# Performance work log

Measured on AMD Instinct MI355X. Metric: run time of the kernel, lower is better.

Reference implementation:

```python
import jax, jax.numpy as jnp
import numpy as np
from jax import lax

B, L, EMB, C, H, NTF = 512, 1024, 4, 64, 64, 200
D2 = 2 * H  # 128, bi-LSTM feature dim


def setup_inputs() -> dict:
    key = jax.random.key(0)
    ks = iter(jax.random.split(key, 48))
    r = lambda shape, s=0.05: jax.random.normal(next(ks), shape, jnp.float32) * s
    inp = {"DNA_x": jax.random.normal(next(ks), (B, L, EMB), jnp.float32)}
    # conv stack: channels 4 -> 64 -> 64, kernel 8
    inp["conv0_w"] = r((C, EMB, 8)); inp["conv0_b"] = r((C,))
    inp["bn0_g"] = 1.0 + r((C,)); inp["bn0_b"] = r((C,))
    inp["bn0_m"] = r((C,)); inp["bn0_v"] = jax.random.uniform(next(ks), (C,), jnp.float32, 0.5, 1.5)
    inp["conv1_w"] = r((C, C, 8)); inp["conv1_b"] = r((C,))
    inp["bn1_g"] = 1.0 + r((C,)); inp["bn1_b"] = r((C,))
    inp["bn1_m"] = r((C,)); inp["bn1_v"] = jax.random.uniform(next(ks), (C,), jnp.float32, 0.5, 1.5)
    # bidirectional LSTM, torch gate order (i, f, g, o)
    for d in ("f", "b"):
        inp[f"wih_{d}"] = r((4 * H, C)); inp[f"whh_{d}"] = r((4 * H, H))
        inp[f"bih_{d}"] = r((4 * H,)); inp[f"bhh_{d}"] = r((4 * H,))
    # Bahdanau attention: W1, W2: 128->128, V: 128->NTF
    inp["W1_w"] = r((D2, D2)); inp["W1_b"] = r((D2,))
    inp["W2_w"] = r((D2, D2)); inp["W2_b"] = r((D2,))
    inp["V_w"] = r((NTF, D2)); inp["V_b"] = r((NTF,))
    # per-TF heads stacked: Linear(128->64), Linear(64->1)
    inp["fc1_w"] = r((NTF, 64, D2)); inp["fc1_b"] = r((NTF, 64))
    inp["fc2_w"] = r((NTF, 64)); inp["fc2_b"] = r((NTF,))
    return inp


def _conv(x, w, b):  # x:[B,Cin,L], w:[Cout,Cin,K]
    y = lax.conv_general_dilated(x, w, (1,), "VALID",
                                 dimension_numbers=("NCH", "OIH", "NCH"))
    return y + b[:, None]


def _bn(x, g, b, m, v):  # eval-mode BatchNorm1d over channel dim
    return (x - m[:, None]) * (g[:, None] / jnp.sqrt(v[:, None] + 1e-5)) + b[:, None]


def _lstm(x, Wih, Whh, bih, bhh):  # x:[B,T,D] -> ([B,T,H], h_T:[B,H])
    Bn = x.shape[0]
    Hh = Whh.shape[1]
    bias = bih + bhh
    def step(carry, xt):
        h, c = carry
        g = xt @ Wih.T + h @ Whh.T + bias
        i, f, gg, o = jnp.split(g, 4, axis=-1)
        c = jax.nn.sigmoid(f) * c + jax.nn.sigmoid(i) * jnp.tanh(gg)
        h = jax.nn.sigmoid(o) * jnp.tanh(c)
        return (h, c), h
    init = (jnp.zeros((Bn, Hh), x.dtype), jnp.zeros((Bn, Hh), x.dtype))
    (hT, _), hs = lax.scan(step, init, jnp.swapaxes(x, 0, 1))
    return jnp.swapaxes(hs, 0, 1), hT


def reference(DNA_x, conv0_w, conv0_b, bn0_g, bn0_b, bn0_m, bn0_v,
              conv1_w, conv1_b, bn1_g, bn1_b, bn1_m, bn1_v,
              wih_f, whh_f, bih_f, bhh_f, wih_b, whh_b, bih_b, bhh_b,
              W1_w, W1_b, W2_w, W2_b, V_w, V_b,
              fc1_w, fc1_b, fc2_w, fc2_b):
    x = jnp.swapaxes(DNA_x, 1, 2)                      # [B,EMB,L]
    x = jax.nn.relu(_bn(_conv(x, conv0_w, conv0_b), bn0_g, bn0_b, bn0_m, bn0_v))
    x = lax.reduce_window(x, -jnp.inf, lax.max, (1, 1, 4), (1, 1, 4), "VALID")
    x = jax.nn.relu(_bn(_conv(x, conv1_w, conv1_b), bn1_g, bn1_b, bn1_m, bn1_v))
    x = jnp.swapaxes(x, 1, 2)                          # [B,T,C], T=247
    hf, hTf = _lstm(x, wih_f, whh_f, bih_f, bhh_f)
    hb, hTb = _lstm(x[:, ::-1, :], wih_b, whh_b, bih_b, bhh_b)
    values = jnp.concatenate([hf, hb[:, ::-1, :]], axis=-1)   # [B,T,2H]
    # torch h_n.view(B, 2H) on [2,B,H]: flat reshape (replicated exactly)
    h_n = jnp.stack([hTf, hTb], axis=0).reshape(values.shape[0], -1)
    # Bahdanau attention with NTF query heads
    score = jnp.tanh(values @ W1_w.T + W1_b + (h_n @ W2_w.T + W2_b)[:, None, :]) @ V_w.T + V_b
    aw = jax.nn.softmax(score, axis=1)                 # [B,T,NTF], softmax over time
    context = jnp.einsum("btd,btk->bkd", values, aw)   # [B,NTF,2H]
    # fused per-TF MLP heads: grouped GEMM over NTF
    h1 = jax.nn.relu(jnp.einsum("bkd,kod->bko", context, fc1_w) + fc1_b)
    out = jnp.einsum("bko,ko->bk", h1, fc2_w) + fc2_b  # [B,NTF]
    return out
```

## Files before the change

kernel.cpp:

```cpp
#include <hip/hip_runtime.h>
#include <math.h>

#define BB 512
#define LL 1024
#define EMB 4
#define CC 64
#define NTF 200
#define TT 247
#define LP 254
#define D2 128

typedef __attribute__((ext_vector_type(8))) short short8;
typedef __attribute__((ext_vector_type(4))) float f32x4;
typedef __attribute__((ext_vector_type(4))) unsigned int uint4v;

__device__ __forceinline__ float sigf(float x) {
  return __builtin_amdgcn_rcpf(1.0f + __expf(-x));
}
__device__ __forceinline__ float tanhff(float x) {
  return 1.0f - 2.0f * __builtin_amdgcn_rcpf(__expf(2.0f * x) + 1.0f);
}

__device__ __forceinline__ void lds_barrier() {
  __builtin_amdgcn_s_waitcnt(0xC07F);
  __builtin_amdgcn_s_barrier();
}

__device__ __forceinline__ unsigned short bfr(float f) {
  unsigned u = __builtin_bit_cast(unsigned, f);
  u += 0x7fffu + ((u >> 16) & 1u);
  return (unsigned short)(u >> 16);
}

__global__ __launch_bounds__(256) void k_cvt(const float* __restrict__ w0,
    const float* __restrict__ w1,
    const float* __restrict__ wihf, const float* __restrict__ whhf,
    const float* __restrict__ wihb, const float* __restrict__ whhb,
    const float* __restrict__ bihf, const float* __restrict__ bhhf,
    const float* __restrict__ bihb, const float* __restrict__ bhhb,
    const float* __restrict__ W1w, const float* __restrict__ Vw,
    const float* __restrict__ f1w,
    unsigned short* __restrict__ wbf0, unsigned short* __restrict__ wbf1r,
    unsigned short* __restrict__ wihbf, unsigned short* __restrict__ whhbf,
    float* __restrict__ lbias,
    unsigned short* __restrict__ W1bf, unsigned short* __restrict__ Vbf,
    unsigned short* __restrict__ f1bf)
{
  int i = blockIdx.x * 256 + threadIdx.x;
  if (i < 2048) wbf0[i] = bfr(w0[i]);
  if (i < 32768) {
    int co = i >> 9, k = (i >> 6) & 7, ci = i & 63;
    wbf1r[i] = bfr(w1[co * 512 + ci * 8 + k]);
  }
  if (i < 16384) {
    wihbf[i] = bfr(wihf[i]);
    wihbf[16384 + i] = bfr(wihb[i]);
    whhbf[i] = bfr(whhf[i]);
    whhbf[16384 + i] = bfr(whhb[i]);
    W1bf[i] = bfr(W1w[i]);
  }
  if (i < 26624) {
    int row = i >> 7;
    Vbf[i] = (row < NTF) ? bfr(Vw[i]) : (unsigned short)0;
  }
  if (i < 256) {
    lbias[i] = bihf[i] + bhhf[i];
    lbias[256 + i] = bihb[i] + bhhb[i];
  }
  if (i < 1638400) f1bf[i] = bfr(f1w[i]);
}

__global__ __launch_bounds__(256) void k_conv0m(const float* __restrict__ x,
    const unsigned short* __restrict__ wbf0,
    const float* __restrict__ b0, const float* __restrict__ g0,
    const float* __restrict__ be0, const float* __restrict__ m0,
    const float* __restrict__ v0, unsigned short* __restrict__ pbf)
{
  int b = blockIdx.x, l0 = blockIdx.y * 64;
  __shared__ float xs[71 * 4];
  __shared__ float sc[64], sb[64];
  int tid = threadIdx.x;
  for (int j = tid; j < 71; j += 256) {
    int l = l0 + j;
    float4 xv = (l < LL) ? *(const float4*)(x + ((size_t)b * LL + l) * EMB)
                         : make_float4(0.f, 0.f, 0.f, 0.f);
    *(float4*)(xs + j * 4) = xv;
  }
  if (tid < 64) {
    float s = g0[tid] * rsqrtf(v0[tid] + 1e-5f);
    sc[tid] = s;
    sb[tid] = (b0[tid] - m0[tid]) * s + be0[tid];
  }
  __syncthreads();
  int w = tid >> 6, lane = tid & 63, nl = lane & 15, quad = lane >> 4;
  const float* ap = xs + (w * 16 + nl) * 4 + quad;
  short8 af;
  #pragma unroll
  for (int j = 0; j < 8; ++j) af[j] = (short)bfr(ap[j * 4]);
  f32x4 acc[4];
  #pragma unroll
  for (int nt = 0; nt < 4; ++nt) {
    short8 bf = __builtin_bit_cast(short8,
        *(const uint4v*)(wbf0 + ((nt * 16 + nl) * 32 + quad * 8)));
    acc[nt] = (f32x4){0.f, 0.f, 0.f, 0.f};
    acc[nt] = __builtin_amdgcn_mfma_f32_16x16x32_bf16(af, bf, acc[nt], 0, 0, 0);
  }
  int t = (l0 >> 2) + w * 4 + quad;
  if (t < LP) {
    #pragma unroll
    for (int nt = 0; nt < 4; ++nt) {
      int c = nt * 16 + nl;
      float scc = sc[c], sbc = sb[c];
      float mx = -1e30f;
      #pragma unroll
      for (int r = 0; r < 4; ++r) mx = fmaxf(mx, acc[nt][r] * scc + sbc);
      pbf[((size_t)b * LP + t) * CC + c] = bfr(fmaxf(mx, 0.0f));
    }
  }
}

__global__ __launch_bounds__(256) void k_conv1m(const unsigned short* __restrict__ pbf,
    const unsigned short* __restrict__ wbf1r,
    const float* __restrict__ b1, const float* __restrict__ g1,
    const float* __restrict__ be1, const float* __restrict__ m1,
    const float* __restrict__ v1, unsigned short* __restrict__ x2bf)
{
  int b = blockIdx.x, t0 = blockIdx.y * 64;
  __shared__ __align__(16) unsigned short ps[71 * 72];
  __shared__ float sc[64], sb[64];
  int tid = threadIdx.x;
  for (int j = tid; j < 71 * 32; j += 256) {
    int tl = j >> 5, cu = j & 31;
    int t = t0 + tl;
    unsigned v = (t < LP) ? *(const unsigned*)(pbf + ((size_t)b * LP + t) * CC + cu * 2) : 0u;
    *(unsigned*)(&ps[tl * 72 + cu * 2]) = v;
  }
  if (tid < 64) {
    float s = g1[tid] * rsqrtf(v1[tid] + 1e-5f);
    sc[tid] = s;
    sb[tid] = (b1[tid] - m1[tid]) * s + be1[tid];
  }
  __syncthreads();
  int w = tid >> 6, lane = tid & 63, nl = lane & 15, quad = lane >> 4;
  int tlb = w * 16 + nl;
  f32x4 acc[4];
  #pragma unroll
  for (int nt = 0; nt < 4; ++nt) acc[nt] = (f32x4){0.f, 0.f, 0.f, 0.f};
  #pragma unroll
  for (int k8 = 0; k8 < 8; ++k8) {
    short8 af0 = __builtin_bit_cast(short8,
        *(const uint4v*)(&ps[(tlb + k8) * 72 + 0 + quad * 8]));
    short8 af1 = __builtin_bit_cast(short8,
        *(const uint4v*)(&ps[(tlb + k8) * 72 + 32 + quad * 8]));
    #pragma unroll
    for (int nt = 0; nt < 4; ++nt) {
      int co = nt * 16 + nl;
      short8 bf0 = __builtin_bit_cast(short8,
          *(const uint4v*)(wbf1r + (size_t)co * 512 + k8 * 64 + 0 + quad * 8));
      short8 bf1 = __builtin_bit_cast(short8,
          *(const uint4v*)(wbf1r + (size_t)co * 512 + k8 * 64 + 32 + quad * 8));
      acc[nt] = __builtin_amdgcn_mfma_f32_16x16x32_bf16(af0, bf0, acc[nt], 0, 0, 0);
      acc[nt] = __builtin_amdgcn_mfma_f32_16x16x32_bf16(af1, bf1, acc[nt], 0, 0, 0);
    }
  }
  #pragma unroll
  for (int nt = 0; nt < 4; ++nt) {
    int c = nt * 16 + nl;
    float scc = sc[c], sbc = sb[c];
    #pragma unroll
    for (int r = 0; r < 4; ++r) {
      int t = t0 + w * 16 + quad * 4 + r;
      if (t < TT)
        x2bf[((size_t)b * TT + t) * CC + c] = bfr(fmaxf(acc[nt][r] * scc + sbc, 0.0f));
    }
  }
}

__global__ __launch_bounds__(256) void k_lstm_m(const unsigned short* __restrict__ x2bf,
    const unsigned short* __restrict__ wihbf, const unsigned short* __restrict__ whhbf,
    const float* __restrict__ lbias,
    unsigned short* __restrict__ values, float* __restrict__ hT)
{
  int b0 = blockIdx.x * 16;
  int dir = blockIdx.y;
  int tid = threadIdx.x;
  int w = tid >> 6, lane = tid & 63, l15 = lane & 15, quad = lane >> 4;
  int h0 = w * 16;
  const unsigned short* wih = wihbf + dir * 16384;
  const unsigned short* whh = whhbf + dir * 16384;

  short8 bx[4][2], bh[4][2];
  float bias_v[4];
  #pragma unroll
  for (int g = 0; g < 4; ++g) {
    int row = g * 64 + h0 + l15;
    #pragma unroll
    for (int k = 0; k < 2; ++k) {
      bx[g][k] = __builtin_bit_cast(short8, *(const uint4v*)(wih + row * 64 + k * 32 + quad * 8));
      bh[g][k] = __builtin_bit_cast(short8, *(const uint4v*)(whh + row * 64 + k * 32 + quad * 8));
    }
    bias_v[g] = lbias[dir * 256 + g * 64 + h0 + l15];
  }

  __shared__ __align__(16) unsigned short xls[2][8][16 * 72];
  __shared__ __align__(16) unsigned short hist[8][16 * 72];
  for (int j = tid; j < 16 * 72; j += 256) hist[7][j] = 0;

  int bl = tid >> 4, d4 = tid & 15;
  const unsigned short* xrow = x2bf + ((size_t)(b0 + bl) * TT) * 64 + d4 * 4;

  uint2 xr[8];
  #pragma unroll
  for (int k = 0; k < 8; ++k) {
    int t = dir ? (TT - 1 - k) : k;
    xr[k] = *(const uint2*)(xrow + (size_t)t * 64);
  }
  #pragma unroll
  for (int k = 0; k < 8; ++k)
    *(uint2*)(&xls[0][k][bl * 72 + d4 * 4]) = xr[k];
  #pragma unroll
  for (int k = 0; k < 8; ++k) {
    int s = 8 + k;
    int t = dir ? (TT - 1 - s) : s;
    xr[k] = *(const uint2*)(xrow + (size_t)t * 64);
  }
  __syncthreads();

  float cst[4] = {0.f, 0.f, 0.f, 0.f};
  for (int c = 0; c < 31; ++c) {
    int buf = c & 1;
    #pragma unroll
    for (int sl = 0; sl < 8; ++sl) {
      int hp = (sl + 7) & 7;
      short8 ax0 = __builtin_bit_cast(short8, *(const uint4v*)(&xls[buf][sl][l15 * 72 + quad * 8]));
      short8 ax1 = __builtin_bit_cast(short8, *(const uint4v*)(&xls[buf][sl][l15 * 72 + 32 + quad * 8]));
      short8 ah0 = __builtin_bit_cast(short8, *(const uint4v*)(&hist[hp][l15 * 72 + quad * 8]));
      short8 ah1 = __builtin_bit_cast(short8, *(const uint4v*)(&hist[hp][l15 * 72 + 32 + quad * 8]));
      f32x4 aX[4], aH[4];
      #pragma unroll
      for (int g = 0; g < 4; ++g) {
        aX[g] = (f32x4){bias_v[g], bias_v[g], bias_v[g], bias_v[g]};
        aX[g] = __builtin_amdgcn_mfma_f32_16x16x32_bf16(ax0, bx[g][0], aX[g], 0, 0, 0);
        aX[g] = __builtin_amdgcn_mfma_f32_16x16x32_bf16(ax1, bx[g][1], aX[g], 0, 0, 0);
        aH[g] = (f32x4){0.f, 0.f, 0.f, 0.f};
        aH[g] = __builtin_amdgcn_mfma_f32_16x16x32_bf16(ah0, bh[g][0], aH[g], 0, 0, 0);
        aH[g] = __builtin_amdgcn_mfma_f32_16x16x32_bf16(ah1, bh[g][1], aH[g], 0, 0, 0);
      }
      #pragma unroll
      for (int r = 0; r < 4; ++r) {
        float ig = sigf(aX[0][r] + aH[0][r]);
        float fg = sigf(aX[1][r] + aH[1][r]);
        float gg = tanhff(aX[2][r] + aH[2][r]);
        float og = sigf(aX[3][r] + aH[3][r]);
        cst[r] = fg * cst[r] + ig * gg;
        float hh = og * tanhff(cst[r]);
        hist[sl][(quad * 4 + r) * 72 + h0 + l15] = bfr(hh);
        if (c == 30 && sl == 6) {
          int bglob = b0 + quad * 4 + r;
          hT[((size_t)dir * BB + bglob) * 64 + h0 + l15] = hh;
        }
      }
      lds_barrier();
    }
    uint4v dv[4];
    #pragma unroll
    for (int i = 0; i < 4; ++i) {
      int flat = i * 256 + tid;
      int sl = flat >> 7, wb = (flat >> 3) & 15, c8 = flat & 7;
      dv[i] = *(const uint4v*)(&hist[sl][wb * 72 + c8 * 8]);
    }
    #pragma unroll
    for (int i = 0; i < 4; ++i) {
      int flat = i * 256 + tid;
      int sl = flat >> 7, wb = (flat >> 3) & 15, c8 = flat & 7;
      int s = c * 8 + sl;
      if (s < TT) {
        int t = dir ? (TT - 1 - s) : s;
        *(uint4v*)(values + ((size_t)(b0 + wb) * TT + t) * D2 + dir * 64 + c8 * 8) = dv[i];
      }
    }
    if (c < 30) {
      #pragma unroll
      for (int k = 0; k < 8; ++k)
        *(uint2*)(&xls[1 - buf][k][bl * 72 + d4 * 4]) = xr[k];
      #pragma unroll
      for (int k = 0; k < 8; ++k) {
        int s2 = (c + 2) * 8 + k;
        if (s2 > TT - 1) s2 = TT - 1;
        int t2 = dir ? (TT - 1 - s2) : s2;
        xr[k] = *(const uint2*)(xrow + (size_t)t2 * 64);
      }
    }
    lds_barrier();
  }
}

__global__ __launch_bounds__(128) void k_q2(const float* __restrict__ hT,
    const float* __restrict__ W2, const float* __restrict__ W2b,
    float* __restrict__ q2)
{
  int b = blockIdx.x;
  int tid = threadIdx.x;
  __shared__ float4 hn4[32];
  ((float*)hn4)[tid] = hT[(size_t)b * 128 + tid];
  __syncthreads();
  const float4* w4 = (const float4*)(W2 + (size_t)tid * 128);
  float a = W2b[tid];
  #pragma unroll
  for (int j = 0; j < 32; ++j) {
    float4 w = w4[j]; float4 h = hn4[j];
    a += w.x * h.x + w.y * h.y + w.z * h.z + w.w * h.w;
  }
  q2[(size_t)b * 128 + tid] = a;
}

__global__ __launch_bounds__(256) void k_score_m(const unsigned short* __restrict__ vbf,
    const unsigned short* __restrict__ W1bf, const float* __restrict__ W1b,
    const float* __restrict__ q2, const unsigned short* __restrict__ Vbf,
    const float* __restrict__ Vb, unsigned short* __restrict__ scoreT)
{
  int b = blockIdx.x, t0 = blockIdx.y * 64;
  int tid = threadIdx.x, w = tid >> 6, lane = tid & 63, l15 = lane & 15, quad = lane >> 4;
  __shared__ unsigned short us[64 * 136];
  __shared__ unsigned short sc2[64 * 213];
  const unsigned short* arow = vbf + ((size_t)b * TT + t0 + w * 16 + l15) * 128;
  short8 ax[4];
  #pragma unroll
  for (int ks = 0; ks < 4; ++ks)
    ax[ks] = __builtin_bit_cast(short8, *(const uint4v*)(arow + ks * 32 + quad * 8));
  #pragma unroll
  for (int nt = 0; nt < 8; ++nt) {
    int n = nt * 16 + l15;
    float base = W1b[n] + q2[(size_t)b * 128 + n];
    f32x4 acc = (f32x4){base, base, base, base};
    #pragma unroll
    for (int ks = 0; ks < 4; ++ks) {
      short8 bf = __builtin_bit_cast(short8,
          *(const uint4v*)(W1bf + (size_t)n * 128 + ks * 32 + quad * 8));
      acc = __builtin_amdgcn_mfma_f32_16x16x32_bf16(ax[ks], bf, acc, 0, 0, 0);
    }
    #pragma unroll
    for (int r = 0; r < 4; ++r)
      us[(w * 16 + quad * 4 + r) * 136 + nt * 16 + l15] = bfr(tanhff(acc[r]));
  }
  __syncthreads();
  short8 au[4];
  #pragma unroll
  for (int ks = 0; ks < 4; ++ks)
    au[ks] = __builtin_bit_cast(short8, *(const uint4v*)(&us[(w * 16 + l15) * 136 + ks * 32 + quad * 8]));
  for (int nt2 = 0; nt2 < 13; ++nt2) {
    int n = nt2 * 16 + l15;
    float b2 = (n < NTF) ? Vb[n] : 0.0f;
    f32x4 a2 = (f32x4){b2, b2, b2, b2};
    #pragma unroll
    for (int ks = 0; ks < 4; ++ks) {
      short8 bf = __builtin_bit_cast(short8,
          *(const uint4v*)(Vbf + (size_t)n * 128 + ks * 32 + quad * 8));
      a2 = __builtin_amdgcn_mfma_f32_16x16x32_bf16(au[ks], bf, a2, 0, 0, 0);
    }
    #pragma unroll
    for (int r = 0; r < 4; ++r) {
      int tl = w * 16 + quad * 4 + r;
      sc2[tl * 213 + n] = bfr(a2[r]);
    }
  }
  __syncthreads();
  int tg = tid & 3;
  #pragma unroll
  for (int pp = 0; pp < 4; ++pp) {
    int nrow = pp * 64 + (tid >> 2);
    if (nrow < NTF) {
      unsigned uu[8];
      #pragma unroll
      for (int k2 = 0; k2 < 8; ++k2) {
        unsigned lo = sc2[(tg * 16 + k2 * 2) * 213 + nrow];
        unsigned hi = sc2[(tg * 16 + k2 * 2 + 1) * 213 + nrow];
        uu[k2] = lo | (hi << 16);
      }
      size_t dst = ((size_t)b * 208 + nrow) * 256 + t0 + tg * 16;
      *(uint4v*)(scoreT + dst) = (uint4v){uu[0], uu[1], uu[2], uu[3]};
      *(uint4v*)(scoreT + dst + 8) = (uint4v){uu[4], uu[5], uu[6], uu[7]};
    }
  }
}

__global__ __launch_bounds__(256) void k_softmax(unsigned short* __restrict__ scoreT,
    float* __restrict__ sinv)
{
  int b = blockIdx.x, nc = blockIdx.y;
  int tid = threadIdx.x;
  int n = nc * 64 + (tid >> 2), tg = tid & 3;
  if (n >= NTF) return;
  unsigned short* row = scoreT + ((size_t)b * 208 + n) * 256 + tg * 64;
  uint4v ld[8];
  #pragma unroll
  for (int i = 0; i < 8; ++i) ld[i] = *(const uint4v*)(row + i * 8);
  float m = -1e30f;
  #pragma unroll
  for (int i = 0; i < 8; ++i) {
    #pragma unroll
    for (int u = 0; u < 4; ++u) {
      unsigned xv = ld[i][u];
      int t0 = tg * 64 + i * 8 + u * 2;
      float a = __builtin_bit_cast(float, xv << 16);
      float c = __builtin_bit_cast(float, xv & 0xffff0000u);
      if (t0 < TT) m = fmaxf(m, a);
      if (t0 + 1 < TT) m = fmaxf(m, c);
    }
  }
  m = fmaxf(m, __shfl_xor(m, 1, 64));
  m = fmaxf(m, __shfl_xor(m, 2, 64));
  float s = 0.0f;
  #pragma unroll
  for (int i = 0; i < 8; ++i) {
    uint4v ov;
    #pragma unroll
    for (int u = 0; u < 4; ++u) {
      unsigned xv = ld[i][u];
      int t0 = tg * 64 + i * 8 + u * 2;
      float a = __builtin_bit_cast(float, xv << 16);
      float c = __builtin_bit_cast(float, xv & 0xffff0000u);
      float ea = (t0 < TT) ? __expf(a - m) : 0.0f;
      float ec = (t0 + 1 < TT) ? __expf(c - m) : 0.0f;
      s += ea + ec;
      ov[u] = (unsigned)bfr(ea) | ((unsigned)bfr(ec) << 16);
    }
    *(uint4v*)(row + i * 8) = ov;
  }
  s += __shfl_xor(s, 1, 64);
  s += __shfl_xor(s, 2, 64);
  if (tg == 0) sinv[(size_t)b * NTF + n] = __builtin_amdgcn_rcpf(s);
}

__global__ __launch_bounds__(256) void k_ctx_m(const unsigned short* __restrict__ vbf,
    const unsigned short* __restrict__ scoreT, const float* __restrict__ sinv,
    unsigned short* __restrict__ ctxbf)
{
  int b = blockIdx.x;
  int tid = threadIdx.x, w = tid >> 6, lane = tid & 63, l15 = lane & 15, quad = lane >> 4;
  __shared__ __align__(16) unsigned short vt[128 * 264];
  __shared__ float sls[208];
  for (int flat = tid; flat < 247 * 64; flat += 256) {
    int t = flat >> 6, dp = flat & 63;
    unsigned v = *(const unsigned*)(vbf + ((size_t)b * TT + t) * D2 + dp * 2);
    vt[(dp * 2) * 264 + t] = (unsigned short)(v & 0xffffu);
    vt[(dp * 2 + 1) * 264 + t] = (unsigned short)(v >> 16);
  }
  for (int j = tid; j < 128 * 9; j += 256) {
    int d = j / 9, t = 247 + (j % 9);
    vt[d * 264 + t] = 0;
  }
  for (int j = tid; j < 208; j += 256) sls[j] = (j < NTF) ? sinv[(size_t)b * NTF + j] : 0.0f;
  __syncthreads();

  const unsigned short* abase = scoreT + (size_t)b * 208 * 256;
  for (int mi = 0; mi < 4; ++mi) {
    int mt = w + 4 * mi;
    if (mt >= 13) continue;
    const unsigned short* arow = abase + (size_t)(mt * 16 + l15) * 256;
    short8 af[8];
    #pragma unroll
    for (int ks = 0; ks < 8; ++ks)
      af[ks] = __builtin_bit_cast(short8, *(const uint4v*)(arow + ks * 32 + quad * 8));
    f32x4 acc[8];
    #pragma unroll
    for (int dt = 0; dt < 8; ++dt) {
      acc[dt] = (f32x4){0.f, 0.f, 0.f, 0.f};
      #pragma unroll
      for (int ks = 0; ks < 8; ++ks) {
        short8 bf = __builtin_bit_cast(short8,
            *(const uint4v*)(&vt[(dt * 16 + l15) * 264 + ks * 32 + quad * 8]));
        acc[dt] = __builtin_amdgcn_mfma_f32_16x16x32_bf16(af[ks], bf, acc[dt], 0, 0, 0);
      }
    }
    #pragma unroll
    for (int r = 0; r < 4; ++r) {
      int n = mt * 16 + quad * 4 + r;
      if (n < NTF) {
        float rs = sls[n];
        #pragma unroll
        for (int dt = 0; dt < 8; ++dt)
          ctxbf[((size_t)b * NTF + n) * D2 + dt * 16 + l15] = bfr(acc[dt][r] * rs);
      }
    }
  }
}

__global__ __launch_bounds__(256) void k_heads_m(const unsigned short* __restrict__ ctxbf,
    const unsigned short* __restrict__ f1bf, const float* __restrict__ fc1b,
    const float* __restrict__ fc2w, const float* __restrict__ fc2b,
    float* __restrict__ out)
{
  int n = blockIdx.x;
  int b0 = blockIdx.y * 128;
  int tid = threadIdx.x, w = tid >> 6, lane = tid & 63, l15 = lane & 15, quad = lane >> 4;
  short8 bfr_[4][4];
  float f1bv[4], f2v[4];
  #pragma unroll
  for (int nt = 0; nt < 4; ++nt) {
    int o = nt * 16 + l15;
    #pragma unroll
    for (int ks = 0; ks < 4; ++ks)
      bfr_[nt][ks] = __builtin_bit_cast(short8,
          *(const uint4v*)(f1bf + ((size_t)n * 64 + o) * 128 + ks * 32 + quad * 8));
    f1bv[nt] = fc1b[n * 64 + o];
    f2v[nt] = fc2w[n * 64 + o];
  }
  float f2b = fc2b[n];
  #pragma unroll
  for (int mi = 0; mi < 2; ++mi) {
    int m16 = (w * 2 + mi) * 16;
    const unsigned short* arow = ctxbf + ((size_t)(b0 + m16 + l15) * NTF + n) * 128;
    short8 af[4];
    #pragma unroll
    for (int ks = 0; ks < 4; ++ks)
      af[ks] = __builtin_bit_cast(short8, *(const uint4v*)(arow + ks * 32 + quad * 8));
    f32x4 acc[4];
    #pragma unroll
    for (int nt = 0; nt < 4; ++nt) {
      acc[nt] = (f32x4){0.f, 0.f, 0.f, 0.f};
      #pragma unroll
      for (int ks = 0; ks < 4; ++ks)
        acc[nt] = __builtin_amdgcn_mfma_f32_16x16x32_bf16(af[ks], bfr_[nt][ks], acc[nt], 0, 0, 0);
    }
    #pragma unroll
    for (int r = 0; r < 4; ++r) {
      float part = 0.0f;
      #pragma unroll
      for (int nt = 0; nt < 4; ++nt)
        part += fmaxf(acc[nt][r] + f1bv[nt], 0.0f) * f2v[nt];
      part += __shfl_xor(part, 1, 64);
      part += __shfl_xor(part, 2, 64);
      part += __shfl_xor(part, 4, 64);
      part += __shfl_xor(part, 8, 64);
      if (l15 == 0) {
        int bb = b0 + m16 + quad * 4 + r;
        out[(size_t)bb * NTF + n] = part + f2b;
      }
    }
  }
}

extern "C" void kernel_launch(void* const* d_in, const int* in_sizes, int n_in,
                              void* d_out, int out_size, void* d_ws, size_t ws_size,
                              hipStream_t stream)
{
  const float* x    = (const float*)d_in[0];
  const float* c0w  = (const float*)d_in[1];
  const float* c0b  = (const float*)d_in[2];
  const float* g0   = (const float*)d_in[3];
  const float* be0  = (const float*)d_in[4];
  const float* m0   = (const float*)d_in[5];
  const float* v0   = (const float*)d_in[6];
  const float* c1w  = (const float*)d_in[7];
  const float* c1b  = (const float*)d_in[8];
  const float* g1   = (const float*)d_in[9];
  const float* be1  = (const float*)d_in[10];
  const float* m1   = (const float*)d_in[11];
  const float* v1   = (const float*)d_in[12];
  const float* wihf = (const float*)d_in[13];
  const float* whhf = (const float*)d_in[14];
  const float* bihf = (const float*)d_in[15];
  const float* bhhf = (const float*)d_in[16];
  const float* wihb = (const float*)d_in[17];
  const float* whhb = (const float*)d_in[18];
  const float* bihb = (const float*)d_in[19];
  const float* bhhb = (const float*)d_in[20];
  const float* W1w  = (const float*)d_in[21];
  const float* W1b  = (const float*)d_in[22];
  const float* W2w  = (const float*)d_in[23];
  const float* W2b  = (const float*)d_in[24];
  const float* Vw   = (const float*)d_in[25];
  const float* Vb   = (const float*)d_in[26];
  const float* f1w  = (const float*)d_in[27];
  const float* f1b  = (const float*)d_in[28];
  const float* f2w  = (const float*)d_in[29];
  const float* f2b  = (const float*)d_in[30];

  float* ws = (float*)d_ws;
  unsigned short* scoreT = (unsigned short*)ws;
  unsigned short* pbf  = (unsigned short*)ws;
  unsigned short* x2bf = (unsigned short*)(ws + 8323072);
  unsigned short* vbf  = (unsigned short*)(ws + 25292800);
  float* hT     = ws + 33387520;
  float* q2     = ws + 33453056;
  float* sinv   = ws + 33518592;
  unsigned short* ctxbf = (unsigned short*)(ws + 33620992);
  unsigned short* wbf0  = (unsigned short*)(ws + 46728192);
  unsigned short* wbf1r = (unsigned short*)(ws + 46729216);
  unsigned short* wihbf = (unsigned short*)(ws + 46745600);
  unsigned short* whhbf = (unsigned short*)(ws + 46761984);
  float* lbias          = ws + 46778368;
  unsigned short* W1bf  = (unsigned short*)(ws + 46778880);
  unsigned short* Vbf   = (unsigned short*)(ws + 46787072);
  unsigned short* f1bf  = (unsigned short*)(ws + 46800384);
  float* out    = (float*)d_out;

  k_cvt<<<dim3(6400), 256, 0, stream>>>(c0w, c1w, wihf, whhf, wihb, whhb,
                                        bihf, bhhf, bihb, bhhb, W1w, Vw, f1w,
                                        wbf0, wbf1r, wihbf, whhbf, lbias, W1bf, Vbf, f1bf);
  k_conv0m<<<dim3(BB, 16), 256, 0, stream>>>(x, wbf0, c0b, g0, be0, m0, v0, pbf);
  k_conv1m<<<dim3(BB, 4), 256, 0, stream>>>(pbf, wbf1r, c1b, g1, be1, m1, v1, x2bf);
  k_lstm_m<<<dim3(BB / 16, 2), 256, 0, stream>>>(x2bf, wihbf, whhbf, lbias, vbf, hT);
  k_q2<<<dim3(BB), 128, 0, stream>>>(hT, W2w, W2b, q2);
  k_score_m<<<dim3(BB, 4), 256, 0, stream>>>(vbf, W1bf, W1b, q2, Vbf, Vb, scoreT);
  k_softmax<<<dim3(BB, 4), 256, 0, stream>>>(scoreT, sinv);
  k_ctx_m<<<dim3(BB), 256, 0, stream>>>(vbf, scoreT, sinv, ctxbf);
  k_heads_m<<<dim3(NTF, 4), 256, 0, stream>>>(ctxbf, f1bf, f1b, f2w, f2b, out);
}
```

Before: 514.9 us.

## Fuse softmax into context GEMM and merge LSTM directions into one block

The separate softmax kernel is removed. The score kernel now writes -inf padding for timesteps past the end, and the context kernel exponentiates the scores while loading them, sums each row with cross-lane shuffles, and scales the output by the reciprocal. The max subtraction is dropped, which relies on scores staying small enough for exp not to overflow. The LSTM now runs both directions in one 512-thread block with per-direction shared-memory buffers, using 4-step chunks instead of 8. This changes the chunk double-buffering and means each block runs 62 chunks instead of 31, with a barrier after every step.

```diff
diff --git a/kernel.cpp b/kernel.cpp
--- a/kernel.cpp
+++ b/kernel.cpp
@@ -176,15 +176,16 @@
   }
 }
 
-__global__ __launch_bounds__(256) void k_lstm_m(const unsigned short* __restrict__ x2bf,
+__global__ __launch_bounds__(512) void k_lstm_m(const unsigned short* __restrict__ x2bf,
     const unsigned short* __restrict__ wihbf, const unsigned short* __restrict__ whhbf,
     const float* __restrict__ lbias,
     unsigned short* __restrict__ values, float* __restrict__ hT)
 {
   int b0 = blockIdx.x * 16;
-  int dir = blockIdx.y;
   int tid = threadIdx.x;
-  int w = tid >> 6, lane = tid & 63, l15 = lane & 15, quad = lane >> 4;
+  int dir = tid >> 8;
+  int t256 = tid & 255;
+  int w = t256 >> 6, lane = tid & 63, l15 = lane & 15, quad = lane >> 4;
   int h0 = w * 16;
   const unsigned short* wih = wihbf + dir * 16384;
   const unsigned short* whh = whhbf + dir * 16384;
@@ -202,40 +203,39 @@
     bias_v[g] = lbias[dir * 256 + g * 64 + h0 + l15];
   }
 
-  __shared__ __align__(16) unsigned short xls[2][8][16 * 72];
-  __shared__ __align__(16) unsigned short hist[8][16 * 72];
-  for (int j = tid; j < 16 * 72; j += 256) hist[7][j] = 0;
-
-  int bl = tid >> 4, d4 = tid & 15;
+  __shared__ __align__(16) unsigned short xls[2][4][16 * 72];
+  __shared__ __align__(16) unsigned short hist[2][4][16 * 72];
+  for (int j = t256; j < 16 * 72; j += 256) hist[dir][3][j] = 0;
+
+  int bl = t256 >> 4, d4 = t256 & 15;
   const unsigned short* xrow = x2bf + ((size_t)(b0 + bl) * TT) * 64 + d4 * 4;
 
-  uint2 xr[8];
-  #pragma unroll
-  for (int k = 0; k < 8; ++k) {
+  uint2 xr[4];
+  #pragma unroll
+  for (int k = 0; k < 4; ++k) {
     int t = dir ? (TT - 1 - k) : k;
     xr[k] = *(const uint2*)(xrow + (size_t)t * 64);
   }
   #pragma unroll
-  for (int k = 0; k < 8; ++k)
-    *(uint2*)(&xls[0][k][bl * 72 + d4 * 4]) = xr[k];
-  #pragma unroll
-  for (int k = 0; k < 8; ++k) {
-    int s = 8 + k;
+  for (int k = 0; k < 4; ++k)
+    *(uint2*)(&xls[dir][k][bl * 72 + d4 * 4]) = xr[k];
+  #pragma unroll
+  for (int k = 0; k < 4; ++k) {
+    int s = 4 + k;
     int t = dir ? (TT - 1 - s) : s;
     xr[k] = *(const uint2*)(xrow + (size_t)t * 64);
   }
   __syncthreads();
 
   float cst[4] = {0.f, 0.f, 0.f, 0.f};
-  for (int c = 0; c < 31; ++c) {
-    int buf = c & 1;
-    #pragma unroll
-    for (int sl = 0; sl < 8; ++sl) {
-      int hp = (sl + 7) & 7;
-      short8 ax0 = __builtin_bit_cast(short8, *(const uint4v*)(&xls[buf][sl][l15 * 72 + quad * 8]));
-      short8 ax1 = __builtin_bit_cast(short8, *(const uint4v*)(&xls[buf][sl][l15 * 72 + 32 + quad * 8]));
-      short8 ah0 = __builtin_bit_cast(short8, *(const uint4v*)(&hist[hp][l15 * 72 + quad * 8]));
-      short8 ah1 = __builtin_bit_cast(short8, *(const uint4v*)(&hist[hp][l15 * 72 + 32 + quad * 8]));
+  for (int c = 0; c < 62; ++c) {
+    #pragma unroll
+    for (int sl = 0; sl < 4; ++sl) {
+      int hp = (sl + 3) & 3;
+      short8 ax0 = __builtin_bit_cast(short8, *(const uint4v*)(&xls[dir][sl][l15 * 72 + quad * 8]));
+      short8 ax1 = __builtin_bit_cast(short8, *(const uint4v*)(&xls[dir][sl][l15 * 72 + 32 + quad * 8]));
+      short8 ah0 = __builtin_bit_cast(short8, *(const uint4v*)(&hist[dir][hp][l15 * 72 + quad * 8]));
+      short8 ah1 = __builtin_bit_cast(short8, *(const uint4v*)(&hist[dir][hp][l15 * 72 + 32 + quad * 8]));
       f32x4 aX[4], aH[4];
       #pragma unroll
       for (int g = 0; g < 4; ++g) {
@@ -254,38 +254,38 @@
         float og = sigf(aX[3][r] + aH[3][r]);
         cst[r] = fg * cst[r] + ig * gg;
         float hh = og * tanhff(cst[r]);
-        hist[sl][(quad * 4 + r) * 72 + h0 + l15] = bfr(hh);
-        if (c == 30 && sl == 6) {
+        hist[dir][sl][(quad * 4 + r) * 72 + h0 + l15] = bfr(hh);
+        if (c == 61 && sl == 2) {
           int bglob = b0 + quad * 4 + r;
           hT[((size_t)dir * BB + bglob) * 64 + h0 + l15] = hh;
         }
       }
       lds_barrier();
     }
-    uint4v dv[4];
-    #pragma unroll
-    for (int i = 0; i < 4; ++i) {
-      int flat = i * 256 + tid;
+    uint4v dv[2];
+    #pragma unroll
+    for (int i = 0; i < 2; ++i) {
+      int flat = i * 256 + t256;
       int sl = flat >> 7, wb = (flat >> 3) & 15, c8 = flat & 7;
-      dv[i] = *(const uint4v*)(&hist[sl][wb * 72 + c8 * 8]);
-    }
-    #pragma unroll
-    for (int i = 0; i < 4; ++i) {
-      int flat = i * 256 + tid;
+      dv[i] = *(const uint4v*)(&hist[dir][sl][wb * 72 + c8 * 8]);
+    }
+    #pragma unroll
+    for (int i = 0; i < 2; ++i) {
+      int flat = i * 256 + t256;
       int sl = flat >> 7, wb = (flat >> 3) & 15, c8 = flat & 7;
-      int s = c * 8 + sl;
+      int s = c * 4 + sl;
       if (s < TT) {
         int t = dir ? (TT - 1 - s) : s;
         *(uint4v*)(values + ((size_t)(b0 + wb) * TT + t) * D2 + dir * 64 + c8 * 8) = dv[i];
       }
     }
-    if (c < 30) {
-      #pragma unroll
-      for (int k = 0; k < 8; ++k)
-        *(uint2*)(&xls[1 - buf][k][bl * 72 + d4 * 4]) = xr[k];
-      #pragma unroll
-      for (int k = 0; k < 8; ++k) {
-        int s2 = (c + 2) * 8 + k;
+    if (c < 61) {
+      #pragma unroll
+      for (int k = 0; k < 4; ++k)
+        *(uint2*)(&xls[dir][k][bl * 72 + d4 * 4]) = xr[k];
+      #pragma unroll
+      for (int k = 0; k < 4; ++k) {
+        int s2 = (c + 2) * 4 + k;
         if (s2 > TT - 1) s2 = TT - 1;
         int t2 = dir ? (TT - 1 - s2) : s2;
         xr[k] = *(const uint2*)(xrow + (size_t)t2 * 64);
@@ -373,8 +373,9 @@
       unsigned uu[8];
       #pragma unroll
       for (int k2 = 0; k2 < 8; ++k2) {
-        unsigned lo = sc2[(tg * 16 + k2 * 2) * 213 + nrow];
-        unsigned hi = sc2[(tg * 16 + k2 * 2 + 1) * 213 + nrow];
+        int ta = t0 + tg * 16 + k2 * 2;
+        unsigned lo = (ta < TT) ? (unsigned)sc2[(tg * 16 + k2 * 2) * 213 + nrow] : 0xFF80u;
+        unsigned hi = (ta + 1 < TT) ? (unsigned)sc2[(tg * 16 + k2 * 2 + 1) * 213 + nrow] : 0xFF80u;
         uu[k2] = lo | (hi << 16);
       }
       size_t dst = ((size_t)b * 208 + nrow) * 256 + t0 + tg * 16;
@@ -384,62 +385,13 @@
   }
 }
 
-__global__ __launch_bounds__(256) void k_softmax(unsigned short* __restrict__ scoreT,
-    float* __restrict__ sinv)
-{
-  int b = blockIdx.x, nc = blockIdx.y;
-  int tid = threadIdx.x;
-  int n = nc * 64 + (tid >> 2), tg = tid & 3;
-  if (n >= NTF) return;
-  unsigned short* row = scoreT + ((size_t)b * 208 + n) * 256 + tg * 64;
-  uint4v ld[8];
-  #pragma unroll
-  for (int i = 0; i < 8; ++i) ld[i] = *(const uint4v*)(row + i * 8);
-  float m = -1e30f;
-  #pragma unroll
-  for (int i = 0; i < 8; ++i) {
-    #pragma unroll
-    for (int u = 0; u < 4; ++u) {
-      unsigned xv = ld[i][u];
-      int t0 = tg * 64 + i * 8 + u * 2;
-      float a = __builtin_bit_cast(float, xv << 16);
-      float c = __builtin_bit_cast(float, xv & 0xffff0000u);
-      if (t0 < TT) m = fmaxf(m, a);
-      if (t0 + 1 < TT) m = fmaxf(m, c);
-    }
-  }
-  m = fmaxf(m, __shfl_xor(m, 1, 64));
-  m = fmaxf(m, __shfl_xor(m, 2, 64));
-  float s = 0.0f;
-  #pragma unroll
-  for (int i = 0; i < 8; ++i) {
-    uint4v ov;
-    #pragma unroll
-    for (int u = 0; u < 4; ++u) {
-      unsigned xv = ld[i][u];
-      int t0 = tg * 64 + i * 8 + u * 2;
-      float a = __builtin_bit_cast(float, xv << 16);
-      float c = __builtin_bit_cast(float, xv & 0xffff0000u);
-      float ea = (t0 < TT) ? __expf(a - m) : 0.0f;
-      float ec = (t0 + 1 < TT) ? __expf(c - m) : 0.0f;
-      s += ea + ec;
-      ov[u] = (unsigned)bfr(ea) | ((unsigned)bfr(ec) << 16);
-    }
-    *(uint4v*)(row + i * 8) = ov;
-  }
-  s += __shfl_xor(s, 1, 64);
-  s += __shfl_xor(s, 2, 64);
-  if (tg == 0) sinv[(size_t)b * NTF + n] = __builtin_amdgcn_rcpf(s);
-}
-
 __global__ __launch_bounds__(256) void k_ctx_m(const unsigned short* __restrict__ vbf,
-    const unsigned short* __restrict__ scoreT, const float* __restrict__ sinv,
+    const unsigned short* __restrict__ scoreT,
     unsigned short* __restrict__ ctxbf)
 {
   int b = blockIdx.x;
   int tid = threadIdx.x, w = tid >> 6, lane = tid & 63, l15 = lane & 15, quad = lane >> 4;
   __shared__ __align__(16) unsigned short vt[128 * 264];
-  __shared__ float sls[208];
   for (int flat = tid; flat < 247 * 64; flat += 256) {
     int t = flat >> 6, dp = flat & 63;
     unsigned v = *(const unsigned*)(vbf + ((size_t)b * TT + t) * D2 + dp * 2);
@@ -450,7 +402,6 @@
     int d = j / 9, t = 247 + (j % 9);
     vt[d * 264 + t] = 0;
   }
-  for (int j = tid; j < 208; j += 256) sls[j] = (j < NTF) ? sinv[(size_t)b * NTF + j] : 0.0f;
   __syncthreads();
 
   const unsigned short* abase = scoreT + (size_t)b * 208 * 256;
@@ -459,9 +410,26 @@
     if (mt >= 13) continue;
     const unsigned short* arow = abase + (size_t)(mt * 16 + l15) * 256;
     short8 af[8];
-    #pragma unroll
-    for (int ks = 0; ks < 8; ++ks)
-      af[ks] = __builtin_bit_cast(short8, *(const uint4v*)(arow + ks * 32 + quad * 8));
+    float ssum = 0.0f;
+    #pragma unroll
+    for (int ks = 0; ks < 8; ++ks) {
+      uint4v raw = *(const uint4v*)(arow + ks * 32 + quad * 8);
+      uint4v pk;
+      #pragma unroll
+      for (int u = 0; u < 4; ++u) {
+        unsigned xv = raw[u];
+        float a = __builtin_bit_cast(float, xv << 16);
+        float c2 = __builtin_bit_cast(float, xv & 0xffff0000u);
+        float ea = __expf(a);
+        float ec = __expf(c2);
+        ssum += ea + ec;
+        pk[u] = (unsigned)bfr(ea) | ((unsigned)bfr(ec) << 16);
+      }
+      af[ks] = __builtin_bit_cast(short8, pk);
+    }
+    ssum += __shfl_xor(ssum, 16, 64);
+    ssum += __shfl_xor(ssum, 32, 64);
+    float rs = __builtin_amdgcn_rcpf(ssum);
     f32x4 acc[8];
     #pragma unroll
     for (int dt = 0; dt < 8; ++dt) {
@@ -476,11 +444,11 @@
     #pragma unroll
     for (int r = 0; r < 4; ++r) {
       int n = mt * 16 + quad * 4 + r;
+      float rr = __shfl(rs, quad * 4 + r, 64);
       if (n < NTF) {
-        float rs = sls[n];
         #pragma unroll
         for (int dt = 0; dt < 8; ++dt)
-          ctxbf[((size_t)b * NTF + n) * D2 + dt * 16 + l15] = bfr(acc[dt][r] * rs);
+          ctxbf[((size_t)b * NTF + n) * D2 + dt * 16 + l15] = bfr(acc[dt][r] * rr);
       }
     }
   }
@@ -584,7 +552,6 @@
   unsigned short* vbf  = (unsigned short*)(ws + 25292800);
   float* hT     = ws + 33387520;
   float* q2     = ws + 33453056;
-  float* sinv   = ws + 33518592;
   unsigned short* ctxbf = (unsigned short*)(ws + 33620992);
   unsigned short* wbf0  = (unsigned short*)(ws + 46728192);
   unsigned short* wbf1r = (unsigned short*)(ws + 46729216);
@@ -601,10 +568,9 @@
                                         wbf0, wbf1r, wihbf, whhbf, lbias, W1bf, Vbf, f1bf);
   k_conv0m<<<dim3(BB, 16), 256, 0, stream>>>(x, wbf0, c0b, g0, be0, m0, v0, pbf);
   k_conv1m<<<dim3(BB, 4), 256, 0, stream>>>(pbf, wbf1r, c1b, g1, be1, m1, v1, x2bf);
-  k_lstm_m<<<dim3(BB / 16, 2), 256, 0, stream>>>(x2bf, wihbf, whhbf, lbias, vbf, hT);
+  k_lstm_m<<<dim3(BB / 16), 512, 0, stream>>>(x2bf, wihbf, whhbf, lbias, vbf, hT);
   k_q2<<<dim3(BB), 128, 0, stream>>>(hT, W2w, W2b, q2);
   k_score_m<<<dim3(BB, 4), 256, 0, stream>>>(vbf, W1bf, W1b, q2, Vbf, Vb, scoreT);
-  k_softmax<<<dim3(BB, 4), 256, 0, stream>>>(scoreT, sinv);
-  k_ctx_m<<<dim3(BB), 256, 0, stream>>>(vbf, scoreT, sinv, ctxbf);
+  k_ctx_m<<<dim3(BB), 256, 0, stream>>>(vbf, scoreT, ctxbf);
   k_heads_m<<<dim3(NTF, 4), 256, 0, stream>>>(ctxbf, f1bf, f1b, f2w, f2b, out);
 }
```

Result: slower. 559.3 us (+8.6%).
